# Kernel tuning notes

Measured on AMD Instinct MI355X. Metric: run time of the kernel, lower is better.

The kernel has to match this reference:

```python
import jax, jax.numpy as jnp
import numpy as np

IN_NC = 32
OUT_NC = 32
EXPAND = 2
HID = IN_NC * EXPAND          # 64
K = 3                         # depthwise kernel
EPS = 1e-5
R1 = IN_NC * HID              # end of pointwise-1 weights
R2 = R1 + HID * K * K         # end of depthwise weights
R3 = R2 + HID * OUT_NC        # total hyper params = 4672


def _bn(t, g, b):
    # BatchNorm2d in training mode over the flattened (b*fh*fw) batch:
    # stats over all axes except the channel axis (axis=3 of [b,fh,fw,C,H,W]).
    ax = (0, 1, 2, 4, 5)
    m = jnp.mean(t, axis=ax, keepdims=True)
    v = jnp.mean((t - m) ** 2, axis=ax, keepdims=True)
    sh = (1, 1, 1, -1, 1, 1)
    return (t - m) * jax.lax.rsqrt(v + EPS) * g.reshape(sh) + b.reshape(sh)


def _relu6(t):
    return jnp.clip(t, 0.0, 6.0)


def setup_inputs() -> dict:
    key = jax.random.key(0)
    k0, k1 = jax.random.split(key)
    x = jax.random.normal(k0, (8, IN_NC, 256, 256), dtype=jnp.float32)
    s = jax.random.normal(k1, (8, R3, 32, 32), dtype=jnp.float32) * 0.1
    return {
        'x': x,
        's': s,
        'gamma1': jnp.ones((HID,), jnp.float32),
        'beta1': jnp.zeros((HID,), jnp.float32),
        'gamma2': jnp.ones((HID,), jnp.float32),
        'beta2': jnp.zeros((HID,), jnp.float32),
        'gamma3': jnp.ones((OUT_NC,), jnp.float32),
        'beta3': jnp.zeros((OUT_NC,), jnp.float32),
    }


def reference(x, s, gamma1, beta1, gamma2, beta2, gamma3, beta3):
    b, c, h, w = x.shape
    fh, fw = s.shape[-2], s.shape[-1]
    ph, pw = h // fh, w // fw          # patch size
    kh, kw = ph + 2, pw + 2            # patch + reflect halo of 1

    # reflect-pad then extract overlapping [kh,kw] patches on a [ph,pw] grid
    xp = jnp.pad(x, ((0, 0), (0, 0), (1, 1), (1, 1)), mode='reflect')
    ri = (jnp.arange(fh) * ph)[:, None] + jnp.arange(kh)   # [fh,kh]
    ci = (jnp.arange(fw) * pw)[:, None] + jnp.arange(kw)   # [fw,kw]
    patches = xp[:, :, ri][:, :, :, :, ci]                 # [b,c,fh,kh,fw,kw]
    patches = patches.transpose(0, 2, 4, 1, 3, 5)          # [b,fh,fw,c,kh,kw]

    sw = s.transpose(0, 2, 3, 1)                           # [b,fh,fw,R3]

    # stage 1: per-patch 1x1 expand conv (in_nc -> hidden)
    w1 = sw[..., :R1].reshape(b, fh, fw, HID, c)
    y = jnp.einsum('bfgoc,bfgchw->bfgohw', w1, patches)    # [b,fh,fw,HID,kh,kw]
    y = _relu6(_bn(y, gamma1, beta1))

    # stage 2: per-patch depthwise 3x3 conv (valid), stride 1 -> [ph,pw]
    w2 = sw[..., R1:R2].reshape(b, fh, fw, HID, K, K)
    z = jnp.zeros((b, fh, fw, HID, ph, pw), y.dtype)
    for u in range(K):
        for v in range(K):
            z = z + w2[..., u, v, None, None] * y[..., u:u + ph, v:v + pw]
    z = _relu6(_bn(z, gamma2, beta2))

    # stage 3: per-patch 1x1 project conv (hidden -> out_nc)
    w3 = sw[..., R2:R3].reshape(b, fh, fw, OUT_NC, HID)
    o = jnp.einsum('bfgoc,bfgcpq->bfgopq', w3, z)          # [b,fh,fw,OUT_NC,ph,pw]
    o = _bn(o, gamma3, beta3)

    # reassemble patches: [b,fh,fw,C,ph,pw] -> [b,C,h,w]
    o = o.transpose(0, 3, 1, 4, 2, 5).reshape(b, OUT_NC, h, w)
    return x + o  # use_res_connect: stride==1 and in_nc==out_nc
```

## Files before the change

### kernel.cpp

```cpp
#include <hip/hip_runtime.h>

#define NT 256

constexpr int R1c = 2048;
constexpr int R2c = 2624;
constexpr float EPSc = 1e-5f;

constexpr int SLOTS1  = 0;
constexpr int SLOTS1Q = 4096;
constexpr int SLOTS2  = 8192;
constexpr int SLOTS2Q = 12288;
constexpr int SLOTS3  = 16384;
constexpr int SLOTS3Q = 18432;
constexpr int FIN1    = 20480;
constexpr int FIN2    = 20608;
constexpr int FIN3    = 20736;
constexpr int STATS_ZERO_FLOATS = 20480;

constexpr size_t ST2_OFF   = 131072;
constexpr size_t ST2_BYTES = 8ull * 1024 * 4672 * 2;
constexpr size_t ZB_OFF    = ST2_OFF + ST2_BYTES;
constexpr size_t ZB_BYTES  = 8192ull * 4096 * 2;
constexpr size_t Y_OFF     = ZB_OFF + ZB_BYTES;
constexpr size_t Y_BYTES   = 8192ull * 13312;
constexpr size_t NEED_Y    = Y_OFF + Y_BYTES;
constexpr size_t OI_OFF    = Y_OFF;

__device__ __forceinline__ ushort f_to_bf16(float f) {
    union { float f; unsigned int i; } v; v.f = f;
    unsigned int r = (v.i + 0x7fffu + ((v.i >> 16) & 1u)) >> 16;
    return (ushort)r;
}
__device__ __forceinline__ float bf16_to_f(ushort u) {
    union { unsigned int i; float f; } v; v.i = ((unsigned int)u) << 16; return v.f;
}
__device__ __forceinline__ float bf16lo_to_f(unsigned int u) {
    union { unsigned int i; float f; } v; v.i = u << 16; return v.f;
}
__device__ __forceinline__ float bf16hi_to_f(unsigned int u) {
    union { unsigned int i; float f; } v; v.i = u & 0xffff0000u; return v.f;
}
__device__ __forceinline__ unsigned int pack_bf16(float lo, float hi) {
    return (unsigned int)f_to_bf16(lo) | ((unsigned int)f_to_bf16(hi) << 16);
}

typedef short bf16x8 __attribute__((ext_vector_type(8)));
typedef float f32x4  __attribute__((ext_vector_type(4)));
union FR { uint4 u4; bf16x8 v; ushort s[8]; };

__device__ __forceinline__ f32x4 mfma16(bf16x8 a, bf16x8 b, f32x4 c) {
    return __builtin_amdgcn_mfma_f32_16x16x32_bf16(a, b, c, 0, 0, 0);
}

__global__ __launch_bounds__(256)
void transpose_s_bf16p(const float* __restrict__ s, ushort* __restrict__ st) {
    __shared__ float tile[64][33];
    const int bi = blockIdx.z;
    const int p0 = blockIdx.x * 64;
    const int q0 = blockIdx.y * 32;
    const int tx = threadIdx.x, ty = threadIdx.y;
    const float* sb = s + (size_t)bi * 4672 * 1024;
    #pragma unroll
    for (int r = ty; r < 64; r += 8)
        tile[r][tx] = sb[(size_t)(p0 + r) * 1024 + q0 + tx];
    __syncthreads();
    unsigned int* stu = (unsigned int*)(st + (size_t)bi * 1024 * 4672);
    #pragma unroll
    for (int rr = ty; rr < 32; rr += 8) {
        int q = q0 + rr;
        unsigned int v = pack_bf16(tile[2*tx][rr], tile[2*tx + 1][rr]);
        stu[((size_t)q * 4672 + p0) / 2 + tx] = v;
    }
}

template<int SY>
__global__ __launch_bounds__(NT, 4)
void k1_mf(const float* __restrict__ x, const ushort* __restrict__ st2,
           ushort* __restrict__ ybuf, float* __restrict__ ws) {
    __shared__ ushort frB[4 * 3584];
    __shared__ float st1[128];
    const int t = threadIdx.x, blk = blockIdx.x;
    const int bi = blk >> 8, f = (blk >> 3) & 31, jb = blk & 7;
    const int g0 = jb * 4, slot = blk & 63;
    const int w = t >> 6, l = t & 63, l15 = l & 15, grp = l >> 4;
    const int patch = bi * 1024 + f * 32 + g0 + w;

    if (t < 128) st1[t] = 0.f;
    {
        int p = t >> 6, e = t & 63;
        if ((e & 15) >= 4)
            ((uint4*)frB)[p * 448 + 384 + e] = make_uint4(0u, 0u, 0u, 0u);
    }
    const ushort* wp = st2 + (size_t)patch * 4672;
    FR aw[4];
    #pragma unroll
    for (int m = 0; m < 4; m++) aw[m].u4 = ((const uint4*)wp)[(m * 16 + l15) * 4 + grp];

    const float* xb = x + (size_t)bi * 32 * 65536;
    for (int i = t; i < 3200; i += NT) {
        int c = i / 100, rem = i - c * 100;
        int r = rem / 10, seg = rem - r * 10;
        int row = f * 8 - 1 + r; row = row < 0 ? -row : (row > 255 ? 510 - row : row);
        int col0 = g0 * 8 - 4 + seg * 4;
        float v4[4];
        if (col0 >= 0 && col0 <= 252) {
            float4 vv = *(const float4*)(xb + (size_t)c * 65536 + row * 256 + col0);
            v4[0] = vv.x; v4[1] = vv.y; v4[2] = vv.z; v4[3] = vv.w;
        } else {
            #pragma unroll
            for (int d = 0; d < 4; d++) {
                int cc = col0 + d; cc = cc < 0 ? -cc : (cc > 255 ? 510 - cc : cc);
                v4[d] = xb[(size_t)c * 65536 + row * 256 + cc];
            }
        }
        int grpc = c >> 3, j = c & 7;
        #pragma unroll
        for (int d = 0; d < 4; d++) {
            int u = col0 + d - g0 * 8;
            ushort hv = f_to_bf16(v4[d]);
            #pragma unroll
            for (int p = 0; p < 4; p++) {
                int pc = u - 8 * p + 1;
                if (pc >= 0 && pc <= 9) {
                    int px = r * 10 + pc;
                    frB[p * 3584 + ((px >> 4) * 64 + grpc * 16 + (px & 15)) * 8 + j] = hv;
                }
            }
        }
    }
    __syncthreads();

    FR b[7];
    const uint4* bp = (const uint4*)(frB + w * 3584);
    #pragma unroll
    for (int n = 0; n < 7; n++) b[n].u4 = bp[n * 64 + l];

    ushort* slice = frB + w * 3584;
    unsigned int* sliceU = (unsigned int*)slice;
    uint4* yb4 = SY ? (((uint4*)ybuf) + (size_t)patch * 832) : nullptr;

    float s4[16], q4[16];
    #pragma unroll
    for (int i = 0; i < 16; i++) { s4[i] = 0.f; q4[i] = 0.f; }
    #pragma unroll
    for (int m = 0; m < 4; m++) {
        #pragma unroll
        for (int n = 0; n < 7; n++) {
            f32x4 z = {0.f, 0.f, 0.f, 0.f};
            f32x4 c = mfma16(aw[m].v, b[n].v, z);
            int px = n * 16 + l15;
            #pragma unroll
            for (int r = 0; r < 4; r++) {
                float v = c[r]; s4[m*4+r] += v; q4[m*4+r] += v * v;
                if (SY && px < 100) slice[(grp * 4 + r) * 106 + px] = f_to_bf16(v);
            }
        }
        if (SY) {
            for (int i = l; i < 208; i += 64) {
                int ch2 = i / 13, sub = i - ch2 * 13;
                int ub = ch2 * 53 + sub * 4;
                yb4[m * 208 + i] = make_uint4(sliceU[ub], sliceU[ub+1], sliceU[ub+2], sliceU[ub+3]);
            }
        }
    }
    #pragma unroll
    for (int i = 0; i < 16; i++) {
        float sm = s4[i], qq = q4[i];
        #pragma unroll
        for (int msk = 1; msk <= 8; msk <<= 1) { sm += __shfl_xor(sm, msk); qq += __shfl_xor(qq, msk); }
        if (l15 == 0) {
            int ch = (i >> 2) * 16 + grp * 4 + (i & 3);
            atomicAdd(&st1[ch], sm);
            atomicAdd(&st1[64 + ch], qq);
        }
    }
    __syncthreads();
    if (t < 64) {
        atomicAdd(&ws[SLOTS1  + t * 64 + slot], st1[t]);
        atomicAdd(&ws[SLOTS1Q + t * 64 + slot], st1[64 + t]);
    }
}

__global__ __launch_bounds__(NT, 4)
void k2_y(const ushort* __restrict__ ybuf, const ushort* __restrict__ st2,
          ushort* __restrict__ zbuf, float* __restrict__ ws) {
    __shared__ ushort slc[4 * 1696];
    __shared__ unsigned int w2L[4 * 288];
    __shared__ float fin_s[128];
    const int t = threadIdx.x, blk = blockIdx.x;
    const int bi = blk >> 8, f = (blk >> 3) & 31, jb = blk & 7;
    const int g0 = jb * 4, slot = blk & 63;
    const int w = t >> 6, l = t & 63;
    const int ch_l = l >> 2, quad = l & 3, p0 = quad * 2;
    const int patch = bi * 1024 + f * 32 + g0 + w;

    if (t < 128) fin_s[t] = ws[FIN1 + t];
    const ushort* wp = st2 + (size_t)patch * 4672;
    for (int k = l; k < 288; k += 64) w2L[w * 288 + k] = ((const unsigned int*)(wp + R1c))[k];
    __syncthreads();

    const uint4* yb4 = ((const uint4*)ybuf) + (size_t)patch * 832;
    ushort* slice = slc + w * 1696;
    unsigned int* sliceU = (unsigned int*)slice;
    const ushort* w2u = (const ushort*)(w2L + w * 288);
    ushort* zp0 = zbuf + (size_t)patch * 4096;
    float zsum[4], zsq[4];

    #pragma unroll
    for (int m = 0; m < 4; m++) {
        for (int i = l; i < 208; i += 64) {
            uint4 v = yb4[m * 208 + i];
            int ch2 = i / 13, sub = i - ch2 * 13;
            int ch = m * 16 + ch2;
            float a1 = fin_s[ch], b1 = fin_s[64 + ch];
            unsigned int uu[4] = {v.x, v.y, v.z, v.w};
            int ub = ch2 * 53 + sub * 4;
            #pragma unroll
            for (int k = 0; k < 4; k++) {
                float lo = fminf(fmaxf(bf16lo_to_f(uu[k]) * a1 + b1, 0.f), 6.f);
                float hi = fminf(fmaxf(bf16hi_to_f(uu[k]) * a1 + b1, 0.f), 6.f);
                sliceU[ub + k] = pack_bf16(lo, hi);
            }
        }
        float yv[4][10];
        #pragma unroll
        for (int rr = 0; rr < 4; rr++) {
            int base = ch_l * 53 + (p0 + rr) * 5;
            #pragma unroll
            for (int k = 0; k < 5; k++) {
                unsigned int u = sliceU[base + k];
                yv[rr][2*k] = bf16lo_to_f(u); yv[rr][2*k+1] = bf16hi_to_f(u);
            }
        }
        float wt[9];
        #pragma unroll
        for (int k = 0; k < 9; k++) wt[k] = bf16_to_f(w2u[(m * 16 + ch_l) * 9 + k]);
        float za[2][8];
        #pragma unroll
        for (int rr = 0; rr < 2; rr++)
            #pragma unroll
            for (int q = 0; q < 8; q++) za[rr][q] = 0.f;
        #pragma unroll
        for (int u = 0; u < 3; u++)
            #pragma unroll
            for (int v = 0; v < 3; v++) {
                float wv = wt[u * 3 + v];
                #pragma unroll
                for (int rr = 0; rr < 2; rr++)
                    #pragma unroll
                    for (int q = 0; q < 8; q++)
                        za[rr][q] += wv * yv[rr + u][q + v];
            }
        float zs = 0.f, zq = 0.f;
        #pragma unroll
        for (int rr = 0; rr < 2; rr++)
            #pragma unroll
            for (int q = 0; q < 8; q++) { float v = za[rr][q]; zs += v; zq += v * v; }
        zsum[m] = zs; zsq[m] = zq;
        ushort* zp = zp0 + (m * 16 + ch_l) * 64 + p0 * 8;
        uint4 pk0, pk1;
        pk0.x = pack_bf16(za[0][0], za[0][1]); pk0.y = pack_bf16(za[0][2], za[0][3]);
        pk0.z = pack_bf16(za[0][4], za[0][5]); pk0.w = pack_bf16(za[0][6], za[0][7]);
        pk1.x = pack_bf16(za[1][0], za[1][1]); pk1.y = pack_bf16(za[1][2], za[1][3]);
        pk1.z = pack_bf16(za[1][4], za[1][5]); pk1.w = pack_bf16(za[1][6], za[1][7]);
        *(uint4*)zp = pk0;
        *(uint4*)(zp + 8) = pk1;
    }
    __syncthreads();
    if (t < 128) fin_s[t] = 0.f;
    __syncthreads();
    #pragma unroll
    for (int m = 0; m < 4; m++) {
        float zs = zsum[m], zq = zsq[m];
        zs += __shfl_xor(zs, 1); zs += __shfl_xor(zs, 2);
        zq += __shfl_xor(zq, 1); zq += __shfl_xor(zq, 2);
        if (quad == 0) {
            atomicAdd(&fin_s[m * 16 + ch_l], zs);
            atomicAdd(&fin_s[64 + m * 16 + ch_l], zq);
        }
    }
    __syncthreads();
    if (t < 64) {
        atomicAdd(&ws[SLOTS2  + t * 64 + slot], fin_s[t]);
        atomicAdd(&ws[SLOTS2Q + t * 64 + slot], fin_s[64 + t]);
    }
}

__global__ __launch_bounds__(NT, 3)
void k2_mf(const float* __restrict__ x, const ushort* __restrict__ st2,
           ushort* __restrict__ zbuf, float* __restrict__ ws) {
    __shared__ ushort frB[4 * 3584];
    __shared__ unsigned int w2L[4 * 288];
    __shared__ float fin_s[128];
    const int t = threadIdx.x, blk = blockIdx.x;
    const int bi = blk >> 8, f = (blk >> 3) & 31, jb = blk & 7;
    const int g0 = jb * 4, slot = blk & 63;
    const int w = t >> 6, l = t & 63, l15 = l & 15, grp = l >> 4;
    const int patch = bi * 1024 + f * 32 + g0 + w;

    if (t < 128) fin_s[t] = ws[FIN1 + t];
    {
        int p = t >> 6, e = t & 63;
        if ((e & 15) >= 4)
            ((uint4*)frB)[p * 448 + 384 + e] = make_uint4(0u, 0u, 0u, 0u);
    }
    const ushort* wp = st2 + (size_t)patch * 4672;
    FR aw[4];
    #pragma unroll
    for (int m = 0; m < 4; m++) aw[m].u4 = ((const uint4*)wp)[(m * 16 + l15) * 4 + grp];
    for (int k = l; k < 288; k += 64) w2L[w * 288 + k] = ((const unsigned int*)(wp + R1c))[k];

    const float* xb = x + (size_t)bi * 32 * 65536;
    for (int i = t; i < 3200; i += NT) {
        int c = i / 100, rem = i - c * 100;
        int r = rem / 10, seg = rem - r * 10;
        int row = f * 8 - 1 + r; row = row < 0 ? -row : (row > 255 ? 510 - row : row);
        int col0 = g0 * 8 - 4 + seg * 4;
        float v4[4];
        if (col0 >= 0 && col0 <= 252) {
            float4 vv = *(const float4*)(xb + (size_t)c * 65536 + row * 256 + col0);
            v4[0] = vv.x; v4[1] = vv.y; v4[2] = vv.z; v4[3] = vv.w;
        } else {
            #pragma unroll
            for (int d = 0; d < 4; d++) {
                int cc = col0 + d; cc = cc < 0 ? -cc : (cc > 255 ? 510 - cc : cc);
                v4[d] = xb[(size_t)c * 65536 + row * 256 + cc];
            }
        }
        int grpc = c >> 3, j = c & 7;
        #pragma unroll
        for (int d = 0; d < 4; d++) {
            int u = col0 + d - g0 * 8;
            ushort hv = f_to_bf16(v4[d]);
            #pragma unroll
            for (int p = 0; p < 4; p++) {
                int pc = u - 8 * p + 1;
                if (pc >= 0 && pc <= 9) {
                    int px = r * 10 + pc;
                    frB[p * 3584 + ((px >> 4) * 64 + grpc * 16 + (px & 15)) * 8 + j] = hv;
                }
            }
        }
    }
    __syncthreads();

    FR b[7];
    const uint4* bp = (const uint4*)(frB + w * 3584);
    #pragma unroll
    for (int n = 0; n < 7; n++) b[n].u4 = bp[n * 64 + l];

    ushort* slice = frB + w * 3584;
    const ushort* w2u = (const ushort*)(w2L + w * 288);
    const int ch_l = l >> 2, quad = l & 3, p0 = quad * 2;
    float zsum[4], zsq[4];
    ushort* zp0 = zbuf + (size_t)patch * 4096;

    #pragma unroll
    for (int m = 0; m < 4; m++) {
        #pragma unroll
        for (int n = 0; n < 7; n++) {
            f32x4 z = {0.f, 0.f, 0.f, 0.f};
            f32x4 c = mfma16(aw[m].v, b[n].v, z);
            int px = n * 16 + l15;
            if (px < 100) {
                #pragma unroll
                for (int r = 0; r < 4; r++) {
                    int ch = m * 16 + grp * 4 + r;
                    float v = fminf(fmaxf(c[r] * fin_s[ch] + fin_s[64 + ch], 0.f), 6.f);
                    slice[(grp * 4 + r) * 102 + px] = f_to_bf16(v);
                }
            }
        }
        float yv[4][10];
        const unsigned int* sl32 = (const unsigned int*)slice;
        #pragma unroll
        for (int rr = 0; rr < 4; rr++) {
            int base = ch_l * 51 + (p0 + rr) * 5;
            #pragma unroll
            for (int k = 0; k < 5; k++) {
                unsigned int u = sl32[base + k];
                yv[rr][2*k] = bf16lo_to_f(u); yv[rr][2*k+1] = bf16hi_to_f(u);
            }
        }
        float wt[9];
        #pragma unroll
        for (int k = 0; k < 9; k++) wt[k] = bf16_to_f(w2u[(m * 16 + ch_l) * 9 + k]);
        float za[2][8];
        #pragma unroll
        for (int rr = 0; rr < 2; rr++)
            #pragma unroll
            for (int q = 0; q < 8; q++) za[rr][q] = 0.f;
        #pragma unroll
        for (int u = 0; u < 3; u++)
            #pragma unroll
            for (int v = 0; v < 3; v++) {
                float wv = wt[u * 3 + v];
                #pragma unroll
                for (int rr = 0; rr < 2; rr++)
                    #pragma unroll
                    for (int q = 0; q < 8; q++)
                        za[rr][q] += wv * yv[rr + u][q + v];
            }
        float zs = 0.f, zq = 0.f;
        #pragma unroll
        for (int rr = 0; rr < 2; rr++)
            #pragma unroll
            for (int q = 0; q < 8; q++) { float v = za[rr][q]; zs += v; zq += v * v; }
        zsum[m] = zs; zsq[m] = zq;
        ushort* zp = zp0 + (m * 16 + ch_l) * 64 + p0 * 8;
        uint4 pk0, pk1;
        pk0.x = pack_bf16(za[0][0], za[0][1]); pk0.y = pack_bf16(za[0][2], za[0][3]);
        pk0.z = pack_bf16(za[0][4], za[0][5]); pk0.w = pack_bf16(za[0][6], za[0][7]);
        pk1.x = pack_bf16(za[1][0], za[1][1]); pk1.y = pack_bf16(za[1][2], za[1][3]);
        pk1.z = pack_bf16(za[1][4], za[1][5]); pk1.w = pack_bf16(za[1][6], za[1][7]);
        *(uint4*)zp = pk0;
        *(uint4*)(zp + 8) = pk1;
    }
    __syncthreads();
    if (t < 128) fin_s[t] = 0.f;
    __syncthreads();
    #pragma unroll
    for (int m = 0; m < 4; m++) {
        float zs = zsum[m], zq = zsq[m];
        zs += __shfl_xor(zs, 1); zs += __shfl_xor(zs, 2);
        zq += __shfl_xor(zq, 1); zq += __shfl_xor(zq, 2);
        if (quad == 0) {
            atomicAdd(&fin_s[m * 16 + ch_l], zs);
            atomicAdd(&fin_s[64 + m * 16 + ch_l], zq);
        }
    }
    __syncthreads();
    if (t < 64) {
        atomicAdd(&ws[SLOTS2  + t * 64 + slot], fin_s[t]);
        atomicAdd(&ws[SLOTS2Q + t * 64 + slot], fin_s[64 + t]);
    }
}

__global__ __launch_bounds__(NT, 4)
void k3_mf(const ushort* __restrict__ zbuf, const ushort* __restrict__ st2,
           ushort* __restrict__ oi, float* __restrict__ ws) {
    __shared__ ushort zL[4 * 4224];
    __shared__ float fin2[128];
    __shared__ float st3[64];
    const int t = threadIdx.x, blk = blockIdx.x;
    const int bi = blk >> 8, f = (blk >> 3) & 31, jb = blk & 7;
    const int g0 = jb * 4, slot = blk & 63;
    const int w = t >> 6, l = t & 63, l15 = l & 15, grp = l >> 4;
    const int patch = bi * 1024 + f * 32 + g0 + w;

    if (t < 128) fin2[t] = ws[FIN2 + t];
    if (t >= 128 && t < 192) st3[t - 128] = 0.f;
    const ushort* wp = st2 + (size_t)patch * 4672;
    FR aw[2][2];
    #pragma unroll
    for (int m = 0; m < 2; m++)
        #pragma unroll
        for (int ks = 0; ks < 2; ks++)
            aw[m][ks].u4 = ((const uint4*)(wp + R2c))[(m * 16 + l15) * 8 + ks * 4 + grp];
    __syncthreads();

    const uint4* zsrc = (const uint4*)(zbuf + (size_t)patch * 4096);
    unsigned int* zd = (unsigned int*)zL;
    #pragma unroll
    for (int it = 0; it < 8; it++) {
        int i = l + 64 * it;
        uint4 v = zsrc[i];
        int ch = i >> 3, px0 = (i & 7) * 8;
        float a2 = fin2[ch], b2 = fin2[64 + ch];
        unsigned int uu[4] = {v.x, v.y, v.z, v.w};
        int base = w * 2112 + (ch * 66 + px0) / 2;
        #pragma unroll
        for (int k = 0; k < 4; k++) {
            float lo = fminf(fmaxf(bf16lo_to_f(uu[k]) * a2 + b2, 0.f), 6.f);
            float hi = fminf(fmaxf(bf16hi_to_f(uu[k]) * a2 + b2, 0.f), 6.f);
            zd[base + k] = pack_bf16(lo, hi);
        }
    }
    FR bfr[2][4];
    #pragma unroll
    for (int ks = 0; ks < 2; ks++)
        #pragma unroll
        for (int n = 0; n < 4; n++)
            #pragma unroll
            for (int j = 0; j < 8; j++)
                bfr[ks][n].s[j] = zL[w * 4224 + (ks * 32 + grp * 8 + j) * 66 + n * 16 + l15];

    float s4[2][4], q4[2][4];
    #pragma unroll
    for (int m = 0; m < 2; m++)
        #pragma unroll
        for (int r = 0; r < 4; r++) { s4[m][r] = 0.f; q4[m][r] = 0.f; }
    #pragma unroll
    for (int m = 0; m < 2; m++)
        #pragma unroll
        for (int n = 0; n < 4; n++) {
            f32x4 z = {0.f, 0.f, 0.f, 0.f};
            f32x4 c = mfma16(aw[m][0].v, bfr[0][n].v, z);
            c = mfma16(aw[m][1].v, bfr[1][n].v, c);
            #pragma unroll
            for (int r = 0; r < 4; r++) {
                float v = c[r];
                s4[m][r] += v; q4[m][r] += v * v;
                int oc = m * 16 + grp * 4 + r;
                int px = n * 16 + l15, p = px >> 3, q = px & 7;
                oi[((size_t)(bi * 32 + oc) * 256 + f * 8 + p) * 256 + (g0 + w) * 8 + q] = f_to_bf16(v);
            }
        }
    #pragma unroll
    for (int m = 0; m < 2; m++)
        #pragma unroll
        for (int r = 0; r < 4; r++) {
            float sm = s4[m][r], qq = q4[m][r];
            #pragma unroll
            for (int msk = 1; msk <= 8; msk <<= 1) { sm += __shfl_xor(sm, msk); qq += __shfl_xor(qq, msk); }
            if (l15 == 0) {
                int oc = m * 16 + grp * 4 + r;
                atomicAdd(&st3[oc], sm);
                atomicAdd(&st3[32 + oc], qq);
            }
        }
    __syncthreads();
    if (t < 32) {
        atomicAdd(&ws[SLOTS3  + t * 64 + slot], st3[t]);
        atomicAdd(&ws[SLOTS3Q + t * 64 + slot], st3[32 + t]);
    }
}

__global__ __launch_bounds__(NT, 8)
void k4_st(const float* __restrict__ x, const float* __restrict__ ws,
           const ushort* __restrict__ oi, float* __restrict__ out) {
    #pragma unroll
    for (int it = 0; it < 8; it++) {
        size_t e = ((size_t)(blockIdx.x * NT + threadIdx.x) + (size_t)it * (2048 * NT)) * 4;
        int oc = (int)((e >> 16) & 31);
        float a3 = ws[FIN3 + oc], b3 = ws[FIN3 + 32 + oc];
        uint2 ov = *(const uint2*)(oi + e);
        float4 xv = *(const float4*)(x + e);
        float4 r;
        r.x = xv.x + bf16lo_to_f(ov.x) * a3 + b3;
        r.y = xv.y + bf16hi_to_f(ov.x) * a3 + b3;
        r.z = xv.z + bf16lo_to_f(ov.y) * a3 + b3;
        r.w = xv.w + bf16hi_to_f(ov.y) * a3 + b3;
        *(float4*)(out + e) = r;
    }
}

__global__ void finalize_k(float* __restrict__ ws, int stage,
                           const float* __restrict__ gamma, const float* __restrict__ beta) {
    int ch = threadIdx.x;
    int nch = (stage == 3) ? 32 : 64;
    if (ch >= nch) return;
    int so = (stage == 1) ? SLOTS1  : (stage == 2) ? SLOTS2  : SLOTS3;
    int sq = (stage == 1) ? SLOTS1Q : (stage == 2) ? SLOTS2Q : SLOTS3Q;
    int fo = (stage == 1) ? FIN1    : (stage == 2) ? FIN2    : FIN3;
    float N = (stage == 1) ? 819200.0f : 524288.0f;
    float sm = 0.f, qq = 0.f;
    for (int j = 0; j < 64; j++) { sm += ws[so + ch*64 + j]; qq += ws[sq + ch*64 + j]; }
    float mean = sm / N;
    float var  = qq / N - mean * mean;
    float rstd = rsqrtf(var + EPSc);
    float a = rstd * gamma[ch];
    ws[fo + ch]       = a;
    ws[fo + nch + ch] = beta[ch] - mean * a;
}

extern "C" void kernel_launch(void* const* d_in, const int* in_sizes, int n_in,
                              void* d_out, int out_size, void* d_ws, size_t ws_size,
                              hipStream_t stream) {
    const float* x  = (const float*)d_in[0];
    const float* s  = (const float*)d_in[1];
    const float* g1 = (const float*)d_in[2];
    const float* b1 = (const float*)d_in[3];
    const float* g2 = (const float*)d_in[4];
    const float* b2 = (const float*)d_in[5];
    const float* g3 = (const float*)d_in[6];
    const float* b3 = (const float*)d_in[7];
    float* out = (float*)d_out;
    float* ws  = (float*)d_ws;

    hipMemsetAsync(d_ws, 0, STATS_ZERO_FLOATS * sizeof(float), stream);

    ushort* st2 = (ushort*)((char*)d_ws + ST2_OFF);
    ushort* zb  = (ushort*)((char*)d_ws + ZB_OFF);
    ushort* yb  = (ushort*)((char*)d_ws + Y_OFF);
    ushort* oi  = (ushort*)((char*)d_ws + OI_OFF);

    const bool big = ws_size >= NEED_Y;

    transpose_s_bf16p<<<dim3(73, 32, 8), dim3(32, 8), 0, stream>>>(s, st2);
    if (big) {
        k1_mf<1><<<2048, NT, 0, stream>>>(x, st2, yb, ws);
        finalize_k<<<1, 64, 0, stream>>>(ws, 1, g1, b1);
        k2_y<<<2048, NT, 0, stream>>>(yb, st2, zb, ws);
    } else {
        k1_mf<0><<<2048, NT, 0, stream>>>(x, st2, nullptr, ws);
        finalize_k<<<1, 64, 0, stream>>>(ws, 1, g1, b1);
        k2_mf<<<2048, NT, 0, stream>>>(x, st2, zb, ws);
    }
    finalize_k<<<1, 64, 0, stream>>>(ws, 2, g2, b2);
    k3_mf<<<2048, NT, 0, stream>>>(zb, st2, oi, ws);
    finalize_k<<<1, 64, 0, stream>>>(ws, 3, g3, b3);
    k4_st<<<2048, NT, 0, stream>>>(x, ws, oi, out);
}
```

Before: 284.8 us.

## Split each patch across two waves to double block count in stages 1-3

The k1, k2 and k3 kernels now handle two patches per block instead of four, with two waves per patch that each own half of the output channels. The grid doubles to 4096 blocks, so there is more parallelism and less shared memory and fewer registers per block. In exchange, each patch's input tile and weights are loaded or staged by more blocks, an extra barrier is added in k1, and k2's stats reduction now uses shared atomics inside the main loop. The old four-patch kernels stay in place for the small-workspace path.

After: 282.4 us. Within noise of the previous version (-0.8%).

```diff
diff --git a/kernel.cpp b/kernel.cpp
--- a/kernel.cpp
+++ b/kernel.cpp
@@ -73,33 +73,35 @@
     }
 }
 
-template<int SY>
-__global__ __launch_bounds__(NT, 4)
-void k1_mf(const float* __restrict__ x, const ushort* __restrict__ st2,
-           ushort* __restrict__ ybuf, float* __restrict__ ws) {
-    __shared__ ushort frB[4 * 3584];
+
+__global__ __launch_bounds__(NT, 2)
+void k1_s(const float* __restrict__ x, const ushort* __restrict__ st2,
+          ushort* __restrict__ ybuf, float* __restrict__ ws) {
+    __shared__ ushort frB[2 * 3584];
     __shared__ float st1[128];
     const int t = threadIdx.x, blk = blockIdx.x;
-    const int bi = blk >> 8, f = (blk >> 3) & 31, jb = blk & 7;
-    const int g0 = jb * 4, slot = blk & 63;
+    const int bi = blk >> 9, f = (blk >> 4) & 31, jb = blk & 15;
+    const int g0 = jb * 2, slot = blk & 63;
     const int w = t >> 6, l = t & 63, l15 = l & 15, grp = l >> 4;
-    const int patch = bi * 1024 + f * 32 + g0 + w;
-
-    if (t < 128) st1[t] = 0.f;
-    {
+    const int pl_ = w >> 1, mh = w & 1;
+    const int patch = bi * 1024 + f * 32 + g0 + pl_;
+
+    if (t < 128) {
+        st1[t] = 0.f;
         int p = t >> 6, e = t & 63;
         if ((e & 15) >= 4)
             ((uint4*)frB)[p * 448 + 384 + e] = make_uint4(0u, 0u, 0u, 0u);
     }
     const ushort* wp = st2 + (size_t)patch * 4672;
-    FR aw[4];
-    #pragma unroll
-    for (int m = 0; m < 4; m++) aw[m].u4 = ((const uint4*)wp)[(m * 16 + l15) * 4 + grp];
+    FR aw[2];
+    #pragma unroll
+    for (int i = 0; i < 2; i++)
+        aw[i].u4 = ((const uint4*)wp)[((mh * 2 + i) * 16 + l15) * 4 + grp];
 
     const float* xb = x + (size_t)bi * 32 * 65536;
-    for (int i = t; i < 3200; i += NT) {
-        int c = i / 100, rem = i - c * 100;
-        int r = rem / 10, seg = rem - r * 10;
+    for (int i = t; i < 1920; i += NT) {
+        int c = i / 60, rem = i - c * 60;
+        int r = rem / 6, seg = rem - r * 6;
         int row = f * 8 - 1 + r; row = row < 0 ? -row : (row > 255 ? 510 - row : row);
         int col0 = g0 * 8 - 4 + seg * 4;
         float v4[4];
@@ -119,7 +121,7 @@
             int u = col0 + d - g0 * 8;
             ushort hv = f_to_bf16(v4[d]);
             #pragma unroll
-            for (int p = 0; p < 4; p++) {
+            for (int p = 0; p < 2; p++) {
                 int pc = u - 8 * p + 1;
                 if (pc >= 0 && pc <= 9) {
                     int px = r * 10 + pc;
@@ -131,45 +133,44 @@
     __syncthreads();
 
     FR b[7];
-    const uint4* bp = (const uint4*)(frB + w * 3584);
+    const uint4* bp = (const uint4*)(frB + pl_ * 3584);
     #pragma unroll
     for (int n = 0; n < 7; n++) b[n].u4 = bp[n * 64 + l];
-
-    ushort* slice = frB + w * 3584;
+    __syncthreads();
+
+    ushort* slice = frB + pl_ * 3584 + mh * 1792;
     unsigned int* sliceU = (unsigned int*)slice;
-    uint4* yb4 = SY ? (((uint4*)ybuf) + (size_t)patch * 832) : nullptr;
-
-    float s4[16], q4[16];
-    #pragma unroll
-    for (int i = 0; i < 16; i++) { s4[i] = 0.f; q4[i] = 0.f; }
-    #pragma unroll
-    for (int m = 0; m < 4; m++) {
+    uint4* yb4 = (uint4*)ybuf + (size_t)patch * 832;
+    float s4[8], q4[8];
+    #pragma unroll
+    for (int i = 0; i < 8; i++) { s4[i] = 0.f; q4[i] = 0.f; }
+    #pragma unroll
+    for (int i = 0; i < 2; i++) {
+        int mm = mh * 2 + i;
         #pragma unroll
         for (int n = 0; n < 7; n++) {
             f32x4 z = {0.f, 0.f, 0.f, 0.f};
-            f32x4 c = mfma16(aw[m].v, b[n].v, z);
+            f32x4 c = mfma16(aw[i].v, b[n].v, z);
             int px = n * 16 + l15;
             #pragma unroll
             for (int r = 0; r < 4; r++) {
-                float v = c[r]; s4[m*4+r] += v; q4[m*4+r] += v * v;
-                if (SY && px < 100) slice[(grp * 4 + r) * 106 + px] = f_to_bf16(v);
-            }
-        }
-        if (SY) {
-            for (int i = l; i < 208; i += 64) {
-                int ch2 = i / 13, sub = i - ch2 * 13;
-                int ub = ch2 * 53 + sub * 4;
-                yb4[m * 208 + i] = make_uint4(sliceU[ub], sliceU[ub+1], sliceU[ub+2], sliceU[ub+3]);
-            }
-        }
-    }
-    #pragma unroll
-    for (int i = 0; i < 16; i++) {
+                float v = c[r]; s4[i*4+r] += v; q4[i*4+r] += v * v;
+                if (px < 100) slice[(grp * 4 + r) * 106 + px] = f_to_bf16(v);
+            }
+        }
+        for (int k = l; k < 208; k += 64) {
+            int ch2 = k / 13, sub = k - ch2 * 13;
+            int ub = ch2 * 53 + sub * 4;
+            yb4[mm * 208 + k] = make_uint4(sliceU[ub], sliceU[ub+1], sliceU[ub+2], sliceU[ub+3]);
+        }
+    }
+    #pragma unroll
+    for (int i = 0; i < 8; i++) {
         float sm = s4[i], qq = q4[i];
         #pragma unroll
         for (int msk = 1; msk <= 8; msk <<= 1) { sm += __shfl_xor(sm, msk); qq += __shfl_xor(qq, msk); }
         if (l15 == 0) {
-            int ch = (i >> 2) * 16 + grp * 4 + (i & 3);
+            int ch = (mh * 2 + (i >> 2)) * 16 + grp * 4 + (i & 3);
             atomicAdd(&st1[ch], sm);
             atomicAdd(&st1[64 + ch], qq);
         }
@@ -181,45 +182,51 @@
     }
 }
 
-__global__ __launch_bounds__(NT, 4)
-void k2_y(const ushort* __restrict__ ybuf, const ushort* __restrict__ st2,
+__global__ __launch_bounds__(NT, 2)
+void k2_s(const ushort* __restrict__ ybuf, const ushort* __restrict__ st2,
           ushort* __restrict__ zbuf, float* __restrict__ ws) {
     __shared__ ushort slc[4 * 1696];
-    __shared__ unsigned int w2L[4 * 288];
+    __shared__ unsigned int w2L[2 * 288];
     __shared__ float fin_s[128];
+    __shared__ float st2s[128];
     const int t = threadIdx.x, blk = blockIdx.x;
-    const int bi = blk >> 8, f = (blk >> 3) & 31, jb = blk & 7;
-    const int g0 = jb * 4, slot = blk & 63;
+    const int bi = blk >> 9, f = (blk >> 4) & 31, jb = blk & 15;
+    const int g0 = jb * 2, slot = blk & 63;
     const int w = t >> 6, l = t & 63;
+    const int pl_ = w >> 1, mh = w & 1;
     const int ch_l = l >> 2, quad = l & 3, p0 = quad * 2;
-    const int patch = bi * 1024 + f * 32 + g0 + w;
-
-    if (t < 128) fin_s[t] = ws[FIN1 + t];
-    const ushort* wp = st2 + (size_t)patch * 4672;
-    for (int k = l; k < 288; k += 64) w2L[w * 288 + k] = ((const unsigned int*)(wp + R1c))[k];
-    __syncthreads();
-
-    const uint4* yb4 = ((const uint4*)ybuf) + (size_t)patch * 832;
+    const int patch = bi * 1024 + f * 32 + g0 + pl_;
+
+    if (t < 128) { fin_s[t] = ws[FIN1 + t]; st2s[t] = 0.f; }
+    for (int k = t; k < 576; k += NT) {
+        int p = (k >= 288) ? 1 : 0;
+        int kk = k - p * 288;
+        const unsigned int* src = (const unsigned int*)(st2 + (size_t)(bi*1024 + f*32 + g0 + p) * 4672 + R1c);
+        w2L[k] = src[kk];
+    }
+    __syncthreads();
+
+    const uint4* yb4 = (const uint4*)ybuf + (size_t)patch * 832;
     ushort* slice = slc + w * 1696;
     unsigned int* sliceU = (unsigned int*)slice;
-    const ushort* w2u = (const ushort*)(w2L + w * 288);
+    const ushort* w2u = (const ushort*)(w2L + pl_ * 288);
     ushort* zp0 = zbuf + (size_t)patch * 4096;
-    float zsum[4], zsq[4];
-
-    #pragma unroll
-    for (int m = 0; m < 4; m++) {
-        for (int i = l; i < 208; i += 64) {
-            uint4 v = yb4[m * 208 + i];
-            int ch2 = i / 13, sub = i - ch2 * 13;
-            int ch = m * 16 + ch2;
+
+    #pragma unroll
+    for (int i = 0; i < 2; i++) {
+        int mm = mh * 2 + i;
+        for (int k = l; k < 208; k += 64) {
+            uint4 v = yb4[mm * 208 + k];
+            int ch2 = k / 13, sub = k - ch2 * 13;
+            int ch = mm * 16 + ch2;
             float a1 = fin_s[ch], b1 = fin_s[64 + ch];
             unsigned int uu[4] = {v.x, v.y, v.z, v.w};
             int ub = ch2 * 53 + sub * 4;
             #pragma unroll
-            for (int k = 0; k < 4; k++) {
-                float lo = fminf(fmaxf(bf16lo_to_f(uu[k]) * a1 + b1, 0.f), 6.f);
-                float hi = fminf(fmaxf(bf16hi_to_f(uu[k]) * a1 + b1, 0.f), 6.f);
-                sliceU[ub + k] = pack_bf16(lo, hi);
+            for (int kk = 0; kk < 4; kk++) {
+                float lo = fminf(fmaxf(bf16lo_to_f(uu[kk]) * a1 + b1, 0.f), 6.f);
+                float hi = fminf(fmaxf(bf16hi_to_f(uu[kk]) * a1 + b1, 0.f), 6.f);
+                sliceU[ub + kk] = pack_bf16(lo, hi);
             }
         }
         float yv[4][10];
@@ -234,7 +241,7 @@
         }
         float wt[9];
         #pragma unroll
-        for (int k = 0; k < 9; k++) wt[k] = bf16_to_f(w2u[(m * 16 + ch_l) * 9 + k]);
+        for (int k = 0; k < 9; k++) wt[k] = bf16_to_f(w2u[(mm * 16 + ch_l) * 9 + k]);
         float za[2][8];
         #pragma unroll
         for (int rr = 0; rr < 2; rr++)
@@ -256,8 +263,13 @@
         for (int rr = 0; rr < 2; rr++)
             #pragma unroll
             for (int q = 0; q < 8; q++) { float v = za[rr][q]; zs += v; zq += v * v; }
-        zsum[m] = zs; zsq[m] = zq;
-        ushort* zp = zp0 + (m * 16 + ch_l) * 64 + p0 * 8;
+        zs += __shfl_xor(zs, 1); zs += __shfl_xor(zs, 2);
+        zq += __shfl_xor(zq, 1); zq += __shfl_xor(zq, 2);
+        if (quad == 0) {
+            atomicAdd(&st2s[mm * 16 + ch_l], zs);
+            atomicAdd(&st2s[64 + mm * 16 + ch_l], zq);
+        }
+        ushort* zp = zp0 + (mm * 16 + ch_l) * 64 + p0 * 8;
         uint4 pk0, pk1;
         pk0.x = pack_bf16(za[0][0], za[0][1]); pk0.y = pack_bf16(za[0][2], za[0][3]);
         pk0.z = pack_bf16(za[0][4], za[0][5]); pk0.w = pack_bf16(za[0][6], za[0][7]);
@@ -267,208 +279,44 @@
         *(uint4*)(zp + 8) = pk1;
     }
     __syncthreads();
-    if (t < 128) fin_s[t] = 0.f;
-    __syncthreads();
-    #pragma unroll
-    for (int m = 0; m < 4; m++) {
-        float zs = zsum[m], zq = zsq[m];
-        zs += __shfl_xor(zs, 1); zs += __shfl_xor(zs, 2);
-        zq += __shfl_xor(zq, 1); zq += __shfl_xor(zq, 2);
-        if (quad == 0) {
-            atomicAdd(&fin_s[m * 16 + ch_l], zs);
-            atomicAdd(&fin_s[64 + m * 16 + ch_l], zq);
-        }
-    }
-    __syncthreads();
     if (t < 64) {
-        atomicAdd(&ws[SLOTS2  + t * 64 + slot], fin_s[t]);
-        atomicAdd(&ws[SLOTS2Q + t * 64 + slot], fin_s[64 + t]);
-    }
-}
-
-__global__ __launch_bounds__(NT, 3)
-void k2_mf(const float* __restrict__ x, const ushort* __restrict__ st2,
-           ushort* __restrict__ zbuf, float* __restrict__ ws) {
-    __shared__ ushort frB[4 * 3584];
-    __shared__ unsigned int w2L[4 * 288];
-    __shared__ float fin_s[128];
-    const int t = threadIdx.x, blk = blockIdx.x;
-    const int bi = blk >> 8, f = (blk >> 3) & 31, jb = blk & 7;
-    const int g0 = jb * 4, slot = blk & 63;
-    const int w = t >> 6, l = t & 63, l15 = l & 15, grp = l >> 4;
-    const int patch = bi * 1024 + f * 32 + g0 + w;
-
-    if (t < 128) fin_s[t] = ws[FIN1 + t];
-    {
-        int p = t >> 6, e = t & 63;
-        if ((e & 15) >= 4)
-            ((uint4*)frB)[p * 448 + 384 + e] = make_uint4(0u, 0u, 0u, 0u);
-    }
-    const ushort* wp = st2 + (size_t)patch * 4672;
-    FR aw[4];
-    #pragma unroll
-    for (int m = 0; m < 4; m++) aw[m].u4 = ((const uint4*)wp)[(m * 16 + l15) * 4 + grp];
-    for (int k = l; k < 288; k += 64) w2L[w * 288 + k] = ((const unsigned int*)(wp + R1c))[k];
-
-    const float* xb = x + (size_t)bi * 32 * 65536;
-    for (int i = t; i < 3200; i += NT) {
-        int c = i / 100, rem = i - c * 100;
-        int r = rem / 10, seg = rem - r * 10;
-        int row = f * 8 - 1 + r; row = row < 0 ? -row : (row > 255 ? 510 - row : row);
-        int col0 = g0 * 8 - 4 + seg * 4;
-        float v4[4];
-        if (col0 >= 0 && col0 <= 252) {
-            float4 vv = *(const float4*)(xb + (size_t)c * 65536 + row * 256 + col0);
-            v4[0] = vv.x; v4[1] = vv.y; v4[2] = vv.z; v4[3] = vv.w;
-        } else {
-            #pragma unroll
-            for (int d = 0; d < 4; d++) {
-                int cc = col0 + d; cc = cc < 0 ? -cc : (cc > 255 ? 510 - cc : cc);
-                v4[d] = xb[(size_t)c * 65536 + row * 256 + cc];
-            }
-        }
-        int grpc = c >> 3, j = c & 7;
-        #pragma unroll
-        for (int d = 0; d < 4; d++) {
-            int u = col0 + d - g0 * 8;
-            ushort hv = f_to_bf16(v4[d]);
-            #pragma unroll
-            for (int p = 0; p < 4; p++) {
-                int pc = u - 8 * p + 1;
-                if (pc >= 0 && pc <= 9) {
-                    int px = r * 10 + pc;
-                    frB[p * 3584 + ((px >> 4) * 64 + grpc * 16 + (px & 15)) * 8 + j] = hv;
-                }
-            }
-        }
-    }
-    __syncthreads();
-
-    FR b[7];
-    const uint4* bp = (const uint4*)(frB + w * 3584);
-    #pragma unroll
-    for (int n = 0; n < 7; n++) b[n].u4 = bp[n * 64 + l];
-
-    ushort* slice = frB + w * 3584;
-    const ushort* w2u = (const ushort*)(w2L + w * 288);
-    const int ch_l = l >> 2, quad = l & 3, p0 = quad * 2;
-    float zsum[4], zsq[4];
-    ushort* zp0 = zbuf + (size_t)patch * 4096;
-
-    #pragma unroll
-    for (int m = 0; m < 4; m++) {
-        #pragma unroll
-        for (int n = 0; n < 7; n++) {
-            f32x4 z = {0.f, 0.f, 0.f, 0.f};
-            f32x4 c = mfma16(aw[m].v, b[n].v, z);
-            int px = n * 16 + l15;
-            if (px < 100) {
-                #pragma unroll
-                for (int r = 0; r < 4; r++) {
-                    int ch = m * 16 + grp * 4 + r;
-                    float v = fminf(fmaxf(c[r] * fin_s[ch] + fin_s[64 + ch], 0.f), 6.f);
-                    slice[(grp * 4 + r) * 102 + px] = f_to_bf16(v);
-                }
-            }
-        }
-        float yv[4][10];
-        const unsigned int* sl32 = (const unsigned int*)slice;
-        #pragma unroll
-        for (int rr = 0; rr < 4; rr++) {
-            int base = ch_l * 51 + (p0 + rr) * 5;
-            #pragma unroll
-            for (int k = 0; k < 5; k++) {
-                unsigned int u = sl32[base + k];
-                yv[rr][2*k] = bf16lo_to_f(u); yv[rr][2*k+1] = bf16hi_to_f(u);
-            }
-        }
-        float wt[9];
-        #pragma unroll
-        for (int k = 0; k < 9; k++) wt[k] = bf16_to_f(w2u[(m * 16 + ch_l) * 9 + k]);
-        float za[2][8];
-        #pragma unroll
-        for (int rr = 0; rr < 2; rr++)
-            #pragma unroll
-            for (int q = 0; q < 8; q++) za[rr][q] = 0.f;
-        #pragma unroll
-        for (int u = 0; u < 3; u++)
-            #pragma unroll
-            for (int v = 0; v < 3; v++) {
-                float wv = wt[u * 3 + v];
-                #pragma unroll
-                for (int rr = 0; rr < 2; rr++)
-                    #pragma unroll
-                    for (int q = 0; q < 8; q++)
-                        za[rr][q] += wv * yv[rr + u][q + v];
-            }
-        float zs = 0.f, zq = 0.f;
-        #pragma unroll
-        for (int rr = 0; rr < 2; rr++)
-            #pragma unroll
-            for (int q = 0; q < 8; q++) { float v = za[rr][q]; zs += v; zq += v * v; }
-        zsum[m] = zs; zsq[m] = zq;
-        ushort* zp = zp0 + (m * 16 + ch_l) * 64 + p0 * 8;
-        uint4 pk0, pk1;
-        pk0.x = pack_bf16(za[0][0], za[0][1]); pk0.y = pack_bf16(za[0][2], za[0][3]);
-        pk0.z = pack_bf16(za[0][4], za[0][5]); pk0.w = pack_bf16(za[0][6], za[0][7]);
-        pk1.x = pack_bf16(za[1][0], za[1][1]); pk1.y = pack_bf16(za[1][2], za[1][3]);
-        pk1.z = pack_bf16(za[1][4], za[1][5]); pk1.w = pack_bf16(za[1][6], za[1][7]);
-        *(uint4*)zp = pk0;
-        *(uint4*)(zp + 8) = pk1;
-    }
-    __syncthreads();
-    if (t < 128) fin_s[t] = 0.f;
-    __syncthreads();
-    #pragma unroll
-    for (int m = 0; m < 4; m++) {
-        float zs = zsum[m], zq = zsq[m];
-        zs += __shfl_xor(zs, 1); zs += __shfl_xor(zs, 2);
-        zq += __shfl_xor(zq, 1); zq += __shfl_xor(zq, 2);
-        if (quad == 0) {
-            atomicAdd(&fin_s[m * 16 + ch_l], zs);
-            atomicAdd(&fin_s[64 + m * 16 + ch_l], zq);
-        }
-    }
-    __syncthreads();
-    if (t < 64) {
-        atomicAdd(&ws[SLOTS2  + t * 64 + slot], fin_s[t]);
-        atomicAdd(&ws[SLOTS2Q + t * 64 + slot], fin_s[64 + t]);
-    }
-}
-
-__global__ __launch_bounds__(NT, 4)
-void k3_mf(const ushort* __restrict__ zbuf, const ushort* __restrict__ st2,
-           ushort* __restrict__ oi, float* __restrict__ ws) {
-    __shared__ ushort zL[4 * 4224];
+        atomicAdd(&ws[SLOTS2  + t * 64 + slot], st2s[t]);
+        atomicAdd(&ws[SLOTS2Q + t * 64 + slot], st2s[64 + t]);
+    }
+}
+
+__global__ __launch_bounds__(NT, 2)
+void k3_s(const ushort* __restrict__ zbuf, const ushort* __restrict__ st2,
+          ushort* __restrict__ oi, float* __restrict__ ws) {
+    __shared__ ushort zL[2 * 4224];
     __shared__ float fin2[128];
     __shared__ float st3[64];
     const int t = threadIdx.x, blk = blockIdx.x;
-    const int bi = blk >> 8, f = (blk >> 3) & 31, jb = blk & 7;
-    const int g0 = jb * 4, slot = blk & 63;
+    const int bi = blk >> 9, f = (blk >> 4) & 31, jb = blk & 15;
+    const int g0 = jb * 2, slot = blk & 63;
     const int w = t >> 6, l = t & 63, l15 = l & 15, grp = l >> 4;
-    const int patch = bi * 1024 + f * 32 + g0 + w;
+    const int pl_ = w >> 1, mh = w & 1;
+    const int patch = bi * 1024 + f * 32 + g0 + pl_;
 
     if (t < 128) fin2[t] = ws[FIN2 + t];
     if (t >= 128 && t < 192) st3[t - 128] = 0.f;
     const ushort* wp = st2 + (size_t)patch * 4672;
-    FR aw[2][2];
-    #pragma unroll
-    for (int m = 0; m < 2; m++)
-        #pragma unroll
-        for (int ks = 0; ks < 2; ks++)
-            aw[m][ks].u4 = ((const uint4*)(wp + R2c))[(m * 16 + l15) * 8 + ks * 4 + grp];
+    FR aw[2];
+    #pragma unroll
+    for (int ks = 0; ks < 2; ks++)
+        aw[ks].u4 = ((const uint4*)(wp + R2c))[(mh * 16 + l15) * 8 + ks * 4 + grp];
     __syncthreads();
 
     const uint4* zsrc = (const uint4*)(zbuf + (size_t)patch * 4096);
     unsigned int* zd = (unsigned int*)zL;
     #pragma unroll
-    for (int it = 0; it < 8; it++) {
-        int i = l + 64 * it;
+    for (int it = 0; it < 4; it++) {
+        int i = mh * 256 + it * 64 + l;
         uint4 v = zsrc[i];
         int ch = i >> 3, px0 = (i & 7) * 8;
         float a2 = fin2[ch], b2 = fin2[64 + ch];
         unsigned int uu[4] = {v.x, v.y, v.z, v.w};
-        int base = w * 2112 + (ch * 66 + px0) / 2;
+        int base = pl_ * 2112 + (ch * 66 + px0) / 2;
         #pragma unroll
         for (int k = 0; k < 4; k++) {
             float lo = fminf(fmaxf(bf16lo_to_f(uu[k]) * a2 + b2, 0.f), 6.f);
@@ -476,6 +324,8 @@
             zd[base + k] = pack_bf16(lo, hi);
         }
     }
+    __syncthreads();
+
     FR bfr[2][4];
     #pragma unroll
     for (int ks = 0; ks < 2; ks++)
@@ -483,42 +333,36 @@
         for (int n = 0; n < 4; n++)
             #pragma unroll
             for (int j = 0; j < 8; j++)
-                bfr[ks][n].s[j] = zL[w * 4224 + (ks * 32 + grp * 8 + j) * 66 + n * 16 + l15];
-
-    float s4[2][4], q4[2][4];
-    #pragma unroll
-    for (int m = 0; m < 2; m++)
-        #pragma unroll
-        for (int r = 0; r < 4; r++) { s4[m][r] = 0.f; q4[m][r] = 0.f; }
-    #pragma unroll
-    for (int m = 0; m < 2; m++)
-        #pragma unroll
-        for (int n = 0; n < 4; n++) {
-            f32x4 z = {0.f, 0.f, 0.f, 0.f};
-            f32x4 c = mfma16(aw[m][0].v, bfr[0][n].v, z);
-            c = mfma16(aw[m][1].v, bfr[1][n].v, c);
-            #pragma unroll
-            for (int r = 0; r < 4; r++) {
-                float v = c[r];
-                s4[m][r] += v; q4[m][r] += v * v;
-                int oc = m * 16 + grp * 4 + r;
-                int px = n * 16 + l15, p = px >> 3, q = px & 7;
-                oi[((size_t)(bi * 32 + oc) * 256 + f * 8 + p) * 256 + (g0 + w) * 8 + q] = f_to_bf16(v);
-            }
-        }
-    #pragma unroll
-    for (int m = 0; m < 2; m++)
+                bfr[ks][n].s[j] = zL[pl_ * 4224 + (ks * 32 + grp * 8 + j) * 66 + n * 16 + l15];
+
+    float s4[4], q4[4];
+    #pragma unroll
+    for (int r = 0; r < 4; r++) { s4[r] = 0.f; q4[r] = 0.f; }
+    #pragma unroll
+    for (int n = 0; n < 4; n++) {
+        f32x4 z = {0.f, 0.f, 0.f, 0.f};
+        f32x4 c = mfma16(aw[0].v, bfr[0][n].v, z);
+        c = mfma16(aw[1].v, bfr[1][n].v, c);
         #pragma unroll
         for (int r = 0; r < 4; r++) {
-            float sm = s4[m][r], qq = q4[m][r];
-            #pragma unroll
-            for (int msk = 1; msk <= 8; msk <<= 1) { sm += __shfl_xor(sm, msk); qq += __shfl_xor(qq, msk); }
-            if (l15 == 0) {
-                int oc = m * 16 + grp * 4 + r;
-                atomicAdd(&st3[oc], sm);
-                atomicAdd(&st3[32 + oc], qq);
-            }
-        }
+            float v = c[r];
+            s4[r] += v; q4[r] += v * v;
+            int oc = mh * 16 + grp * 4 + r;
+            int px = n * 16 + l15, p = px >> 3, q = px & 7;
+            oi[((size_t)(bi * 32 + oc) * 256 + f * 8 + p) * 256 + (g0 + pl_) * 8 + q] = f_to_bf16(v);
+        }
+    }
+    #pragma unroll
+    for (int r = 0; r < 4; r++) {
+        float sm = s4[r], qq = q4[r];
+        #pragma unroll
+        for (int msk = 1; msk <= 8; msk <<= 1) { sm += __shfl_xor(sm, msk); qq += __shfl_xor(qq, msk); }
+        if (l15 == 0) {
+            int oc = mh * 16 + grp * 4 + r;
+            atomicAdd(&st3[oc], sm);
+            atomicAdd(&st3[32 + oc], qq);
+        }
+    }
     __syncthreads();
     if (t < 32) {
         atomicAdd(&ws[SLOTS3  + t * 64 + slot], st3[t]);
@@ -564,6 +408,336 @@
     ws[fo + nch + ch] = beta[ch] - mean * a;
 }
 
+__global__ __launch_bounds__(NT, 4)
+void k1_mf(const float* __restrict__ x, const ushort* __restrict__ st2,
+           float* __restrict__ ws) {
+    __shared__ ushort frB[4 * 3584];
+    __shared__ float st1[128];
+    const int t = threadIdx.x, blk = blockIdx.x;
+    const int bi = blk >> 8, f = (blk >> 3) & 31, jb = blk & 7;
+    const int g0 = jb * 4, slot = blk & 63;
+    const int w = t >> 6, l = t & 63, l15 = l & 15, grp = l >> 4;
+
+    if (t < 128) st1[t] = 0.f;
+    {
+        int p = t >> 6, e = t & 63;
+        if ((e & 15) >= 4)
+            ((uint4*)frB)[p * 448 + 384 + e] = make_uint4(0u, 0u, 0u, 0u);
+    }
+    const ushort* wp = st2 + (size_t)(bi * 1024 + f * 32 + g0 + w) * 4672;
+    FR aw[4];
+    #pragma unroll
+    for (int m = 0; m < 4; m++) aw[m].u4 = ((const uint4*)wp)[(m * 16 + l15) * 4 + grp];
+
+    const float* xb = x + (size_t)bi * 32 * 65536;
+    for (int i = t; i < 3200; i += NT) {
+        int c = i / 100, rem = i - c * 100;
+        int r = rem / 10, seg = rem - r * 10;
+        int row = f * 8 - 1 + r; row = row < 0 ? -row : (row > 255 ? 510 - row : row);
+        int col0 = g0 * 8 - 4 + seg * 4;
+        float v4[4];
+        if (col0 >= 0 && col0 <= 252) {
+            float4 vv = *(const float4*)(xb + (size_t)c * 65536 + row * 256 + col0);
+            v4[0] = vv.x; v4[1] = vv.y; v4[2] = vv.z; v4[3] = vv.w;
+        } else {
+            #pragma unroll
+            for (int d = 0; d < 4; d++) {
+                int cc = col0 + d; cc = cc < 0 ? -cc : (cc > 255 ? 510 - cc : cc);
+                v4[d] = xb[(size_t)c * 65536 + row * 256 + cc];
+            }
+        }
+        int grpc = c >> 3, j = c & 7;
+        #pragma unroll
+        for (int d = 0; d < 4; d++) {
+            int u = col0 + d - g0 * 8;
+            ushort hv = f_to_bf16(v4[d]);
+            #pragma unroll
+            for (int p = 0; p < 4; p++) {
+                int pc = u - 8 * p + 1;
+                if (pc >= 0 && pc <= 9) {
+                    int px = r * 10 + pc;
+                    frB[p * 3584 + ((px >> 4) * 64 + grpc * 16 + (px & 15)) * 8 + j] = hv;
+                }
+            }
+        }
+    }
+    __syncthreads();
+
+    FR b[7];
+    const uint4* bp = (const uint4*)(frB + w * 3584);
+    #pragma unroll
+    for (int n = 0; n < 7; n++) b[n].u4 = bp[n * 64 + l];
+    float s4[16], q4[16];
+    #pragma unroll
+    for (int i = 0; i < 16; i++) { s4[i] = 0.f; q4[i] = 0.f; }
+    #pragma unroll
+    for (int m = 0; m < 4; m++) {
+        #pragma unroll
+        for (int n = 0; n < 7; n++) {
+            f32x4 z = {0.f, 0.f, 0.f, 0.f};
+            f32x4 c = mfma16(aw[m].v, b[n].v, z);
+            #pragma unroll
+            for (int r = 0; r < 4; r++) { float v = c[r]; s4[m*4+r] += v; q4[m*4+r] += v * v; }
+        }
+    }
+    #pragma unroll
+    for (int i = 0; i < 16; i++) {
+        float sm = s4[i], qq = q4[i];
+        #pragma unroll
+        for (int msk = 1; msk <= 8; msk <<= 1) { sm += __shfl_xor(sm, msk); qq += __shfl_xor(qq, msk); }
+        if (l15 == 0) {
+            int ch = (i >> 2) * 16 + grp * 4 + (i & 3);
+            atomicAdd(&st1[ch], sm);
+            atomicAdd(&st1[64 + ch], qq);
+        }
+    }
+    __syncthreads();
+    if (t < 64) {
+        atomicAdd(&ws[SLOTS1  + t * 64 + slot], st1[t]);
+        atomicAdd(&ws[SLOTS1Q + t * 64 + slot], st1[64 + t]);
+    }
+}
+
+__global__ __launch_bounds__(NT, 3)
+void k2_mf(const float* __restrict__ x, const ushort* __restrict__ st2,
+           ushort* __restrict__ zbuf, float* __restrict__ ws) {
+    __shared__ ushort frB[4 * 3584];
+    __shared__ unsigned int w2L[4 * 288];
+    __shared__ float fin_s[128];
+    const int t = threadIdx.x, blk = blockIdx.x;
+    const int bi = blk >> 8, f = (blk >> 3) & 31, jb = blk & 7;
+    const int g0 = jb * 4, slot = blk & 63;
+    const int w = t >> 6, l = t & 63, l15 = l & 15, grp = l >> 4;
+    const int patch = bi * 1024 + f * 32 + g0 + w;
+
+    if (t < 128) fin_s[t] = ws[FIN1 + t];
+    {
+        int p = t >> 6, e = t & 63;
+        if ((e & 15) >= 4)
+            ((uint4*)frB)[p * 448 + 384 + e] = make_uint4(0u, 0u, 0u, 0u);
+    }
+    const ushort* wp = st2 + (size_t)patch * 4672;
+    FR aw[4];
+    #pragma unroll
+    for (int m = 0; m < 4; m++) aw[m].u4 = ((const uint4*)wp)[(m * 16 + l15) * 4 + grp];
+    for (int k = l; k < 288; k += 64) w2L[w * 288 + k] = ((const unsigned int*)(wp + R1c))[k];
+
+    const float* xb = x + (size_t)bi * 32 * 65536;
+    for (int i = t; i < 3200; i += NT) {
+        int c = i / 100, rem = i - c * 100;
+        int r = rem / 10, seg = rem - r * 10;
+        int row = f * 8 - 1 + r; row = row < 0 ? -row : (row > 255 ? 510 - row : row);
+        int col0 = g0 * 8 - 4 + seg * 4;
+        float v4[4];
+        if (col0 >= 0 && col0 <= 252) {
+            float4 vv = *(const float4*)(xb + (size_t)c * 65536 + row * 256 + col0);
+            v4[0] = vv.x; v4[1] = vv.y; v4[2] = vv.z; v4[3] = vv.w;
+        } else {
+            #pragma unroll
+            for (int d = 0; d < 4; d++) {
+                int cc = col0 + d; cc = cc < 0 ? -cc : (cc > 255 ? 510 - cc : cc);
+                v4[d] = xb[(size_t)c * 65536 + row * 256 + cc];
+            }
+        }
+        int grpc = c >> 3, j = c & 7;
+        #pragma unroll
+        for (int d = 0; d < 4; d++) {
+            int u = col0 + d - g0 * 8;
+            ushort hv = f_to_bf16(v4[d]);
+            #pragma unroll
+            for (int p = 0; p < 4; p++) {
+                int pc = u - 8 * p + 1;
+                if (pc >= 0 && pc <= 9) {
+                    int px = r * 10 + pc;
+                    frB[p * 3584 + ((px >> 4) * 64 + grpc * 16 + (px & 15)) * 8 + j] = hv;
+                }
+            }
+        }
+    }
+    __syncthreads();
+
+    FR b[7];
+    const uint4* bp = (const uint4*)(frB + w * 3584);
+    #pragma unroll
+    for (int n = 0; n < 7; n++) b[n].u4 = bp[n * 64 + l];
+
+    ushort* slice = frB + w * 3584;
+    const ushort* w2u = (const ushort*)(w2L + w * 288);
+    const int ch_l = l >> 2, quad = l & 3, p0 = quad * 2;
+    float zsum[4], zsq[4];
+    ushort* zp0 = zbuf + (size_t)patch * 4096;
+
+    #pragma unroll
+    for (int m = 0; m < 4; m++) {
+        #pragma unroll
+        for (int n = 0; n < 7; n++) {
+            f32x4 z = {0.f, 0.f, 0.f, 0.f};
+            f32x4 c = mfma16(aw[m].v, b[n].v, z);
+            int px = n * 16 + l15;
+            if (px < 100) {
+                #pragma unroll
+                for (int r = 0; r < 4; r++) {
+                    int ch = m * 16 + grp * 4 + r;
+                    float v = fminf(fmaxf(c[r] * fin_s[ch] + fin_s[64 + ch], 0.f), 6.f);
+                    slice[(grp * 4 + r) * 102 + px] = f_to_bf16(v);
+                }
+            }
+        }
+        float yv[4][10];
+        const unsigned int* sl32 = (const unsigned int*)slice;
+        #pragma unroll
+        for (int rr = 0; rr < 4; rr++) {
+            int base = ch_l * 51 + (p0 + rr) * 5;
+            #pragma unroll
+            for (int k = 0; k < 5; k++) {
+                unsigned int u = sl32[base + k];
+                yv[rr][2*k] = bf16lo_to_f(u); yv[rr][2*k+1] = bf16hi_to_f(u);
+            }
+        }
+        float wt[9];
+        #pragma unroll
+        for (int k = 0; k < 9; k++) wt[k] = bf16_to_f(w2u[(m * 16 + ch_l) * 9 + k]);
+        float za[2][8];
+        #pragma unroll
+        for (int rr = 0; rr < 2; rr++)
+            #pragma unroll
+            for (int q = 0; q < 8; q++) za[rr][q] = 0.f;
+        #pragma unroll
+        for (int u = 0; u < 3; u++)
+            #pragma unroll
+            for (int v = 0; v < 3; v++) {
+                float wv = wt[u * 3 + v];
+                #pragma unroll
+                for (int rr = 0; rr < 2; rr++)
+                    #pragma unroll
+                    for (int q = 0; q < 8; q++)
+                        za[rr][q] += wv * yv[rr + u][q + v];
+            }
+        float zs = 0.f, zq = 0.f;
+        #pragma unroll
+        for (int rr = 0; rr < 2; rr++)
+            #pragma unroll
+            for (int q = 0; q < 8; q++) { float v = za[rr][q]; zs += v; zq += v * v; }
+        zsum[m] = zs; zsq[m] = zq;
+        ushort* zp = zp0 + (m * 16 + ch_l) * 64 + p0 * 8;
+        uint4 pk0, pk1;
+        pk0.x = pack_bf16(za[0][0], za[0][1]); pk0.y = pack_bf16(za[0][2], za[0][3]);
+        pk0.z = pack_bf16(za[0][4], za[0][5]); pk0.w = pack_bf16(za[0][6], za[0][7]);
+        pk1.x = pack_bf16(za[1][0], za[1][1]); pk1.y = pack_bf16(za[1][2], za[1][3]);
+        pk1.z = pack_bf16(za[1][4], za[1][5]); pk1.w = pack_bf16(za[1][6], za[1][7]);
+        *(uint4*)zp = pk0;
+        *(uint4*)(zp + 8) = pk1;
+    }
+    __syncthreads();
+    if (t < 128) fin_s[t] = 0.f;
+    __syncthreads();
+    #pragma unroll
+    for (int m = 0; m < 4; m++) {
+        float zs = zsum[m], zq = zsq[m];
+        zs += __shfl_xor(zs, 1); zs += __shfl_xor(zs, 2);
+        zq += __shfl_xor(zq, 1); zq += __shfl_xor(zq, 2);
+        if (quad == 0) {
+            atomicAdd(&fin_s[m * 16 + ch_l], zs);
+            atomicAdd(&fin_s[64 + m * 16 + ch_l], zq);
+        }
+    }
+    __syncthreads();
+    if (t < 64) {
+        atomicAdd(&ws[SLOTS2  + t * 64 + slot], fin_s[t]);
+        atomicAdd(&ws[SLOTS2Q + t * 64 + slot], fin_s[64 + t]);
+    }
+}
+
+__global__ __launch_bounds__(NT, 4)
+void k3_mf(const ushort* __restrict__ zbuf, const ushort* __restrict__ st2,
+           ushort* __restrict__ oi, float* __restrict__ ws) {
+    __shared__ ushort zL[4 * 4224];
+    __shared__ float fin2[128];
+    __shared__ float st3[64];
+    const int t = threadIdx.x, blk = blockIdx.x;
+    const int bi = blk >> 8, f = (blk >> 3) & 31, jb = blk & 7;
+    const int g0 = jb * 4, slot = blk & 63;
+    const int w = t >> 6, l = t & 63, l15 = l & 15, grp = l >> 4;
+    const int patch = bi * 1024 + f * 32 + g0 + w;
+
+    if (t < 128) fin2[t] = ws[FIN2 + t];
+    if (t >= 128 && t < 192) st3[t - 128] = 0.f;
+    const ushort* wp = st2 + (size_t)patch * 4672;
+    FR aw[2][2];
+    #pragma unroll
+    for (int m = 0; m < 2; m++)
+        #pragma unroll
+        for (int ks = 0; ks < 2; ks++)
+            aw[m][ks].u4 = ((const uint4*)(wp + R2c))[(m * 16 + l15) * 8 + ks * 4 + grp];
+    __syncthreads();
+
+    const uint4* zsrc = (const uint4*)(zbuf + (size_t)patch * 4096);
+    unsigned int* zd = (unsigned int*)zL;
+    #pragma unroll
+    for (int it = 0; it < 8; it++) {
+        int i = l + 64 * it;
+        uint4 v = zsrc[i];
+        int ch = i >> 3, px0 = (i & 7) * 8;
+        float a2 = fin2[ch], b2 = fin2[64 + ch];
+        unsigned int uu[4] = {v.x, v.y, v.z, v.w};
+        int base = w * 2112 + (ch * 66 + px0) / 2;
+        #pragma unroll
+        for (int k = 0; k < 4; k++) {
+            float lo = fminf(fmaxf(bf16lo_to_f(uu[k]) * a2 + b2, 0.f), 6.f);
+            float hi = fminf(fmaxf(bf16hi_to_f(uu[k]) * a2 + b2, 0.f), 6.f);
+            zd[base + k] = pack_bf16(lo, hi);
+        }
+    }
+    FR bfr[2][4];
+    #pragma unroll
+    for (int ks = 0; ks < 2; ks++)
+        #pragma unroll
+        for (int n = 0; n < 4; n++)
+            #pragma unroll
+            for (int j = 0; j < 8; j++)
+                bfr[ks][n].s[j] = zL[w * 4224 + (ks * 32 + grp * 8 + j) * 66 + n * 16 + l15];
+
+    float s4[2][4], q4[2][4];
+    #pragma unroll
+    for (int m = 0; m < 2; m++)
+        #pragma unroll
+        for (int r = 0; r < 4; r++) { s4[m][r] = 0.f; q4[m][r] = 0.f; }
+    #pragma unroll
+    for (int m = 0; m < 2; m++)
+        #pragma unroll
+        for (int n = 0; n < 4; n++) {
+            f32x4 z = {0.f, 0.f, 0.f, 0.f};
+            f32x4 c = mfma16(aw[m][0].v, bfr[0][n].v, z);
+            c = mfma16(aw[m][1].v, bfr[1][n].v, c);
+            #pragma unroll
+            for (int r = 0; r < 4; r++) {
+                float v = c[r];
+                s4[m][r] += v; q4[m][r] += v * v;
+                int oc = m * 16 + grp * 4 + r;
+                int px = n * 16 + l15, p = px >> 3, q = px & 7;
+                oi[((size_t)(bi * 32 + oc) * 256 + f * 8 + p) * 256 + (g0 + w) * 8 + q] = f_to_bf16(v);
+            }
+        }
+    #pragma unroll
+    for (int m = 0; m < 2; m++)
+        #pragma unroll
+        for (int r = 0; r < 4; r++) {
+            float sm = s4[m][r], qq = q4[m][r];
+            #pragma unroll
+            for (int msk = 1; msk <= 8; msk <<= 1) { sm += __shfl_xor(sm, msk); qq += __shfl_xor(qq, msk); }
+            if (l15 == 0) {
+                int oc = m * 16 + grp * 4 + r;
+                atomicAdd(&st3[oc], sm);
+                atomicAdd(&st3[32 + oc], qq);
+            }
+        }
+    __syncthreads();
+    if (t < 32) {
+        atomicAdd(&ws[SLOTS3  + t * 64 + slot], st3[t]);
+        atomicAdd(&ws[SLOTS3Q + t * 64 + slot], st3[32 + t]);
+    }
+}
+
 extern "C" void kernel_launch(void* const* d_in, const int* in_sizes, int n_in,
                               void* d_out, int out_size, void* d_ws, size_t ws_size,
                               hipStream_t stream) {
@@ -589,16 +763,18 @@
 
     transpose_s_bf16p<<<dim3(73, 32, 8), dim3(32, 8), 0, stream>>>(s, st2);
     if (big) {
-        k1_mf<1><<<2048, NT, 0, stream>>>(x, st2, yb, ws);
+        k1_s<<<4096, NT, 0, stream>>>(x, st2, yb, ws);
         finalize_k<<<1, 64, 0, stream>>>(ws, 1, g1, b1);
-        k2_y<<<2048, NT, 0, stream>>>(yb, st2, zb, ws);
+        k2_s<<<4096, NT, 0, stream>>>(yb, st2, zb, ws);
+        finalize_k<<<1, 64, 0, stream>>>(ws, 2, g2, b2);
+        k3_s<<<4096, NT, 0, stream>>>(zb, st2, oi, ws);
     } else {
-        k1_mf<0><<<2048, NT, 0, stream>>>(x, st2, nullptr, ws);
+        k1_mf<<<2048, NT, 0, stream>>>(x, st2, ws);
         finalize_k<<<1, 64, 0, stream>>>(ws, 1, g1, b1);
         k2_mf<<<2048, NT, 0, stream>>>(x, st2, zb, ws);
-    }
-    finalize_k<<<1, 64, 0, stream>>>(ws, 2, g2, b2);
-    k3_mf<<<2048, NT, 0, stream>>>(zb, st2, oi, ws);
+        finalize_k<<<1, 64, 0, stream>>>(ws, 2, g2, b2);
+        k3_mf<<<2048, NT, 0, stream>>>(zb, st2, oi, ws);
+    }
     finalize_k<<<1, 64, 0, stream>>>(ws, 3, g3, b3);
     k4_st<<<2048, NT, 0, stream>>>(x, ws, oi, out);
 }
```
